# Performance work log

Hardware: AMD Instinct MI355X
Metric: run time of the kernel (lower is better)

Reference implementation:

```python
import jax, jax.numpy as jnp
import numpy as np

D_MODEL = 256
D_FF = 2048
H_HEADS = 8
N_LEVELS = 5
N_POINTS = 4
SPATIAL = [(128, 128), (64, 64), (32, 32), (16, 16), (8, 8)]
LV = sum(h * w for h, w in SPATIAL)  # 21824
LQ = 900
B = 8
D_HEAD = D_MODEL // H_HEADS


def _layer_norm(x, g, b, eps=1e-5):
    m = jnp.mean(x, -1, keepdims=True)
    v = jnp.mean((x - m) ** 2, -1, keepdims=True)
    return (x - m) * jax.lax.rsqrt(v + eps) * g + b


def _ms_deform_core(value, loc, attn_w):
    # value [B,Lv,H,D]; loc [B,Lq,H,L,P,2] normalized in [0,1]; attn_w [B,Lq,H,L,P]
    Bn, Lq = loc.shape[0], loc.shape[1]
    Dh = value.shape[-1]
    out = jnp.zeros((Bn, H_HEADS, Lq, Dh), value.dtype)
    start = 0
    for l, (Hh, Ww) in enumerate(SPATIAL):
        v = value[:, start:start + Hh * Ww].transpose(0, 2, 1, 3)  # [B,H,HW,D]
        start += Hh * Ww
        xy = loc[:, :, :, l]  # [B,Lq,H,P,2]
        # grid_sample align_corners=False: pixel = norm*size - 0.5
        x = xy[..., 0] * Ww - 0.5
        y = xy[..., 1] * Hh - 0.5
        x0 = jnp.floor(x); y0 = jnp.floor(y)
        fx = x - x0; fy = y - y0
        samp = jnp.zeros((Bn, H_HEADS, Lq * N_POINTS, Dh), value.dtype)
        corners = ((0, 0, (1 - fx) * (1 - fy)), (1, 0, fx * (1 - fy)),
                   (0, 1, (1 - fx) * fy), (1, 1, fx * fy))
        for dx, dy, wgt in corners:
            xc = x0 + dx; yc = y0 + dy
            valid = (xc >= 0) & (xc < Ww) & (yc >= 0) & (yc < Hh)  # zero padding
            idx = (jnp.clip(yc, 0, Hh - 1) * Ww + jnp.clip(xc, 0, Ww - 1)).astype(jnp.int32)
            wv = jnp.where(valid, wgt, 0.0)
            idx_r = idx.transpose(0, 2, 1, 3).reshape(Bn, H_HEADS, Lq * N_POINTS)
            wv_r = wv.transpose(0, 2, 1, 3).reshape(Bn, H_HEADS, Lq * N_POINTS)
            g = jnp.take_along_axis(v, idx_r[..., None], axis=2)  # [B,H,LqP,D]
            samp = samp + wv_r[..., None] * g
        samp = samp.reshape(Bn, H_HEADS, Lq, N_POINTS, Dh)
        aw = attn_w[:, :, :, l].transpose(0, 2, 1, 3)  # [B,H,Lq,P]
        out = out + (samp * aw[..., None]).sum(axis=3)
    return out.transpose(0, 2, 1, 3).reshape(Bn, Lq, H_HEADS * Dh)


def _forward(tgt, tgt_query_pos, tgt_reference_points, memory,
             sa_w_q, sa_b_q, sa_w_k, sa_b_k, sa_w_v, sa_b_v, sa_w_o, sa_b_o,
             ca_w_off, ca_b_off, ca_w_attn, ca_b_attn, ca_w_val, ca_b_val, ca_w_out, ca_b_out,
             ffn_w1, ffn_b1, ffn_w2, ffn_b2,
             ln1_g, ln1_b, ln2_g, ln2_b, ln3_g, ln3_b):
    Lq, Bn, C = tgt.shape
    scale = float(1.0 / np.sqrt(D_HEAD))
    # ---- self-attention (torch nn.MultiheadAttention, seq-first) ----
    qk = tgt + tgt_query_pos
    def heads(x):
        return x.reshape(Lq, Bn, H_HEADS, D_HEAD).transpose(1, 2, 0, 3)
    q = heads(qk @ sa_w_q + sa_b_q) * scale
    k = heads(qk @ sa_w_k + sa_b_k)
    v = heads(tgt @ sa_w_v + sa_b_v)
    attn = jax.nn.softmax(jnp.einsum('bhqd,bhkd->bhqk', q, k), axis=-1)
    o = jnp.einsum('bhqk,bhkd->bhqd', attn, v).transpose(2, 0, 1, 3).reshape(Lq, Bn, C)
    tgt = _layer_norm(tgt + (o @ sa_w_o + sa_b_o), ln2_g, ln2_b)
    # ---- multi-scale deformable cross-attention ----
    qb = (tgt + tgt_query_pos).transpose(1, 0, 2)            # [B,Lq,C]
    ref = tgt_reference_points.transpose(1, 0, 2, 3)         # [B,Lq,L,2]
    value = (memory.transpose(1, 0, 2) @ ca_w_val + ca_b_val).reshape(Bn, LV, H_HEADS, D_HEAD)
    off = (qb @ ca_w_off + ca_b_off).reshape(Bn, Lq, H_HEADS, N_LEVELS, N_POINTS, 2)
    aw = jax.nn.softmax((qb @ ca_w_attn + ca_b_attn).reshape(Bn, Lq, H_HEADS, N_LEVELS * N_POINTS), axis=-1)
    aw = aw.reshape(Bn, Lq, H_HEADS, N_LEVELS, N_POINTS)
    offset_normalizer = jnp.asarray([[w, h] for h, w in SPATIAL], tgt.dtype)  # (W,H) per level
    loc = ref[:, :, None, :, None, :] + off / offset_normalizer[None, None, None, :, None, :]
    samp = _ms_deform_core(value, loc, aw)                   # [B,Lq,C]
    o = (samp @ ca_w_out + ca_b_out).transpose(1, 0, 2)
    tgt = _layer_norm(tgt + o, ln1_g, ln1_b)
    # ---- FFN ----
    h = jax.nn.relu(tgt @ ffn_w1 + ffn_b1)
    tgt = _layer_norm(tgt + (h @ ffn_w2 + ffn_b2), ln3_g, ln3_b)
    return tgt


def setup_inputs() -> dict:
    key = jax.random.key(0)
    ks = iter(jax.random.split(key, 64))
    f32 = jnp.float32
    def nrm(shape, s=1.0):
        return (s * jax.random.normal(next(ks), shape)).astype(f32)
    inp = {}
    inp['tgt'] = nrm((LQ, B, D_MODEL))
    inp['tgt_query_pos'] = nrm((LQ, B, D_MODEL))
    inp['tgt_reference_points'] = jax.random.uniform(next(ks), (LQ, B, N_LEVELS, 2), f32)
    inp['memory'] = nrm((LV, B, D_MODEL))
    inp['memory_spatial_shapes'] = jnp.asarray(SPATIAL, jnp.int32)
    inp['memory_level_start_index'] = jnp.asarray(np.cumsum([0] + [h * w for h, w in SPATIAL[:-1]]), jnp.int32)
    for n, shp in [('sa_w_q', (D_MODEL, D_MODEL)), ('sa_w_k', (D_MODEL, D_MODEL)),
                   ('sa_w_v', (D_MODEL, D_MODEL)), ('sa_w_o', (D_MODEL, D_MODEL)),
                   ('ca_w_off', (D_MODEL, H_HEADS * N_LEVELS * N_POINTS * 2)),
                   ('ca_w_attn', (D_MODEL, H_HEADS * N_LEVELS * N_POINTS)),
                   ('ca_w_val', (D_MODEL, D_MODEL)), ('ca_w_out', (D_MODEL, D_MODEL)),
                   ('ffn_w1', (D_MODEL, D_FF)), ('ffn_w2', (D_FF, D_MODEL))]:
        inp[n] = nrm(shp, 0.02)
    for n, d in [('sa_b_q', D_MODEL), ('sa_b_k', D_MODEL), ('sa_b_v', D_MODEL), ('sa_b_o', D_MODEL),
                 ('ca_b_off', H_HEADS * N_LEVELS * N_POINTS * 2), ('ca_b_attn', H_HEADS * N_LEVELS * N_POINTS),
                 ('ca_b_val', D_MODEL), ('ca_b_out', D_MODEL), ('ffn_b1', D_FF), ('ffn_b2', D_MODEL)]:
        inp[n] = jnp.zeros((d,), f32)
    for n in ['ln1', 'ln2', 'ln3']:
        inp[n + '_g'] = jnp.ones((D_MODEL,), f32)
        inp[n + '_b'] = jnp.zeros((D_MODEL,), f32)
    return inp


def reference(tgt, tgt_query_pos, tgt_reference_points, memory,
              memory_spatial_shapes, memory_level_start_index,
              sa_w_q, sa_b_q, sa_w_k, sa_b_k, sa_w_v, sa_b_v, sa_w_o, sa_b_o,
              ca_w_off, ca_b_off, ca_w_attn, ca_b_attn, ca_w_val, ca_b_val, ca_w_out, ca_b_out,
              ffn_w1, ffn_b1, ffn_w2, ffn_b2,
              ln1_g, ln1_b, ln2_g, ln2_b, ln3_g, ln3_b):
    # spatial shapes / level start index are static metadata (SPATIAL), kept for API parity
    return _forward(tgt, tgt_query_pos, tgt_reference_points, memory,
                    sa_w_q, sa_b_q, sa_w_k, sa_b_k, sa_w_v, sa_b_v, sa_w_o, sa_b_o,
                    ca_w_off, ca_b_off, ca_w_attn, ca_b_attn, ca_w_val, ca_b_val, ca_w_out, ca_b_out,
                    ffn_w1, ffn_b1, ffn_w2, ffn_b2,
                    ln1_g, ln1_b, ln2_g, ln2_b, ln3_g, ln3_b)
```

## Files before the change

kernel.cpp:

```cpp
#include <hip/hip_runtime.h>
#include <hip/hip_bf16.h>
#include <type_traits>

#define LQ    900
#define BSZ   8
#define ROWS  (LQ*BSZ)
#define CDIM  256
#define QKS   512
#define OAS   480
#define NH    8
#define DH    32
#define LVTOT 21824
#define VROWS (LVTOT*BSZ)
#define DFF   2048

typedef unsigned short u16;
typedef short short8 __attribute__((ext_vector_type(8)));
typedef float f32x4 __attribute__((ext_vector_type(4)));

__device__ __forceinline__ u16 f2bf(float f) {
    __hip_bfloat16 h = __float2bfloat16(f);
    return *reinterpret_cast<u16*>(&h);
}
#define ATTN_SCALE 0.1767766952966369f
#define SWZ(r) (((r) & 3) ^ (((r) >> 2) & 3))

__global__ __launch_bounds__(256) void addvec_kernel(const float* __restrict__ a,
                                                     const float* __restrict__ b,
                                                     float* __restrict__ c, int n4) {
    int i = blockIdx.x * 256 + threadIdx.x;
    if (i < n4) {
        float4 x = reinterpret_cast<const float4*>(a)[i];
        float4 y = reinterpret_cast<const float4*>(b)[i];
        reinterpret_cast<float4*>(c)[i] = make_float4(x.x+y.x, x.y+y.y, x.z+y.z, x.w+y.w);
    }
}

struct PrepArgs {
    const float* Wq; const float* Wk; const float* Wv; const float* Wo;
    const float* Wval; const float* Wout; const float* Woff; const float* Watt;
    const float* W1; const float* W2;
    u16* WqkT; u16* WvT; u16* WoT; u16* WvalT; u16* WoutT; u16* WoaT; u16* W1T; u16* W2T;
    const float* bq; const float* bk; const float* boff; const float* batt;
    float* bqk; float* boa;
};
__global__ __launch_bounds__(256) void prep_kernel(PrepArgs a) {
    __shared__ float t[32][33];
    const int id = blockIdx.x;
    if (id == 1528) {
        const int tx = threadIdx.x;
        if (tx < 256) { a.bqk[tx] = a.bq[tx] * ATTN_SCALE; a.bqk[256 + tx] = a.bk[tx]; }
        for (int i = tx; i < 320; i += 256) a.boa[i] = a.boff[i];
        if (tx < 160) a.boa[320 + tx] = a.batt[tx];
        return;
    }
    const float* W; u16* Wt; int K = 256, N = 256, nx = 8; float scale = 1.f; int r;
    if      (id < 64)   { W = a.Wq;   Wt = a.WqkT;           scale = ATTN_SCALE; r = id; }
    else if (id < 128)  { W = a.Wk;   Wt = a.WqkT + 256*256; r = id - 64; }
    else if (id < 192)  { W = a.Wv;   Wt = a.WvT;            r = id - 128; }
    else if (id < 256)  { W = a.Wo;   Wt = a.WoT;            r = id - 192; }
    else if (id < 320)  { W = a.Wval; Wt = a.WvalT;          r = id - 256; }
    else if (id < 384)  { W = a.Wout; Wt = a.WoutT;          r = id - 320; }
    else if (id < 464)  { W = a.Woff; Wt = a.WoaT;           N = 320; nx = 10; r = id - 384; }
    else if (id < 504)  { W = a.Watt; Wt = a.WoaT + 320*256; N = 160; nx = 5;  r = id - 464; }
    else if (id < 1016) { W = a.W1;   Wt = a.W1T;            N = 2048; nx = 64; r = id - 504; }
    else                { W = a.W2;   Wt = a.W2T;            K = 2048; N = 256; nx = 8; r = id - 1016; }
    const int n0 = (r % nx) * 32, k0 = (r / nx) * 32;
    const int tx = threadIdx.x & 31, ty = threadIdx.x >> 5;
    #pragma unroll
    for (int rr = ty; rr < 32; rr += 8)
        t[rr][tx] = W[(size_t)(k0 + rr) * N + n0 + tx];
    __syncthreads();
    #pragma unroll
    for (int rr = ty; rr < 32; rr += 8)
        Wt[(size_t)(n0 + rr) * K + k0 + tx] = f2bf(t[tx][rr] * scale);
}

template<typename AT, int RELU, typename OutT>
__device__ __forceinline__ void gemm_body(const AT* __restrict__ A,
                                          const u16* __restrict__ Wt,
                                          const float* __restrict__ bias,
                                          OutT* __restrict__ C,
                                          int M, int N, int K,
                                          int m0, int n0, int tid, u16* S) {
    const int lane = tid & 63;
    const int w = tid >> 6;
    const int wr = w >> 2, wc = w & 3;
    const int lr = lane & 15, lg = lane >> 4;
    const int sr = tid >> 2, sc = tid & 3;
    const int ns = K >> 5;
    const int arow = (m0 + sr < M) ? (m0 + sr) : (M - 1);
    int brow = n0 + sr; if (brow > N - 1) brow = N - 1;
    const u16* Bsrc = Wt + (size_t)brow * K + ((sc ^ SWZ(sr)) << 3);
    u16* Bdst = S + 8192 + ((tid & ~63) << 3);

    f32x4 acc[4][2] = {};
    float4 fal[4], fah[4];
    short8 fab[4];

#define LOADA(I, KK) do { \
    if constexpr (std::is_same<AT, float>::value) { \
        const float4* s_ = reinterpret_cast<const float4*>((const float*)A + (size_t)arow*K + (KK)*32 + sc*8); \
        fal[I] = s_[0]; fah[I] = s_[1]; \
    } else { \
        fab[I] = *reinterpret_cast<const short8*>((const u16*)A + (size_t)arow*K + (KK)*32 + sc*8); \
    } } while (0)

#define STAGEB(BUF, KK) \
    __builtin_amdgcn_global_load_lds((const __attribute__((address_space(1))) void*)(Bsrc + (size_t)(KK)*32), \
        (__attribute__((address_space(3))) void*)(Bdst + (BUF)*4096), 16, 0, 0)

#define WRITEA(BUF, I) do { \
    u16 t_[8]; \
    if constexpr (std::is_same<AT, float>::value) { \
        t_[0]=f2bf(fal[I].x); t_[1]=f2bf(fal[I].y); t_[2]=f2bf(fal[I].z); t_[3]=f2bf(fal[I].w); \
        t_[4]=f2bf(fah[I].x); t_[5]=f2bf(fah[I].y); t_[6]=f2bf(fah[I].z); t_[7]=f2bf(fah[I].w); \
    } else { *reinterpret_cast<short8*>(t_) = fab[I]; } \
    *reinterpret_cast<uint4*>(&S[(BUF)*4096 + sr*32 + ((sc ^ SWZ(sr)) * 8)]) = *reinterpret_cast<const uint4*>(t_); \
    } while (0)

#define WAITVM() do { \
    if constexpr (std::is_same<AT, float>::value) asm volatile("s_waitcnt vmcnt(7)" ::: "memory"); \
    else asm volatile("s_waitcnt vmcnt(5)" ::: "memory"); } while (0)

#define COMPUTE(CUR, BB) do { \
    short8 af_[4], bf_[2]; \
    _Pragma("unroll") for (int i = 0; i < 4; ++i) { \
        const int r_ = wr*64 + i*16 + lr; \
        af_[i] = *reinterpret_cast<const short8*>(&S[(CUR)*4096 + r_*32 + ((lg ^ SWZ(r_)) * 8)]); } \
    _Pragma("unroll") for (int j = 0; j < 2; ++j) { \
        const int rb_ = wc*32 + j*16 + lr; \
        bf_[j] = *reinterpret_cast<const short8*>(&S[8192 + (BB)*4096 + rb_*32 + ((lg ^ SWZ(rb_)) * 8)]); } \
    _Pragma("unroll") for (int i = 0; i < 4; ++i) \
        _Pragma("unroll") for (int j = 0; j < 2; ++j) \
            acc[i][j] = __builtin_amdgcn_mfma_f32_16x16x32_bf16(af_[i], bf_[j], acc[i][j], 0, 0, 0); \
    } while (0)

#define STEP(c) do { \
    asm volatile("s_waitcnt lgkmcnt(0)" ::: "memory"); \
    __builtin_amdgcn_s_barrier(); \
    int kp_ = k4 + (c) + 3; if (kp_ > ns - 1) kp_ = ns - 1; \
    LOADA(((c)+3)&3, kp_); STAGEB(((c)+3)&3, kp_); \
    WAITVM(); \
    WRITEA(((c)+1)&1, ((c)+1)&3); \
    COMPUTE((c)&1, (c)&3); } while (0)

    LOADA(0, 0); STAGEB(0, 0);
    LOADA(1, 1); STAGEB(1, 1);
    LOADA(2, 2); STAGEB(2, 2);
    WAITVM();
    WRITEA(0, 0);

    for (int q = 0; q < (ns >> 2); ++q) {
        const int k4 = q << 2;
        STEP(0); STEP(1); STEP(2); STEP(3);
    }
    asm volatile("s_waitcnt vmcnt(0) lgkmcnt(0)" ::: "memory");
    __builtin_amdgcn_s_barrier();

#undef LOADA
#undef STAGEB
#undef WRITEA
#undef WAITVM
#undef COMPUTE
#undef STEP

    if constexpr (std::is_same<OutT, float>::value) {
        #pragma unroll
        for (int j = 0; j < 2; ++j) {
            const int col = n0 + wc*32 + j*16 + lr;
            if (col >= N) continue;
            const float bcol = bias[col];
            #pragma unroll
            for (int i = 0; i < 4; ++i) {
                #pragma unroll
                for (int r = 0; r < 4; ++r) {
                    const int row = m0 + wr*64 + i*16 + lg*4 + r;
                    if (row >= M) continue;
                    float v = acc[i][j][r] + bcol;
                    if (RELU) v = fmaxf(v, 0.f);
                    C[(size_t)row * N + col] = v;
                }
            }
        }
    } else {
        u16* Ct = S;
        #pragma unroll
        for (int j = 0; j < 2; ++j) {
            const int col = wc*32 + j*16 + lr;
            const float bcol = bias[n0 + col];
            #pragma unroll
            for (int i = 0; i < 4; ++i)
                #pragma unroll
                for (int r = 0; r < 4; ++r) {
                    float v = acc[i][j][r] + bcol;
                    if (RELU) v = fmaxf(v, 0.f);
                    Ct[(wr*64 + i*16 + lg*4 + r)*128 + col] = f2bf(v);
                }
        }
        __syncthreads();
        #pragma unroll
        for (int it = 0; it < 4; ++it) {
            const int idx = it*512 + tid;
            const int row = idx >> 4, cc = idx & 15;
            if (m0 + row < M)
                *reinterpret_cast<uint4*>(&C[(size_t)(m0 + row) * N + n0 + cc*8]) =
                    *reinterpret_cast<const uint4*>(&Ct[row*128 + cc*8]);
        }
    }
}

template<typename AT, int RELU, typename OutT>
__global__ __launch_bounds__(512) void gemm_mfma(const AT* __restrict__ A,
                                                 const u16* __restrict__ Wt,
                                                 const float* __restrict__ bias,
                                                 OutT* __restrict__ C, int M, int N, int K) {
    __shared__ __align__(16) u16 S[24576];
    gemm_body<AT, RELU, OutT>(A, Wt, bias, C, M, N, K,
                              blockIdx.y * 128, blockIdx.x * 128, threadIdx.x, S);
}

__global__ __launch_bounds__(512) void mgemm3_kernel(
        const float* __restrict__ memory, const u16* __restrict__ WvalT, const float* __restrict__ bval, u16* __restrict__ Cval,
        const float* __restrict__ qkin,   const u16* __restrict__ WqkT,  const float* __restrict__ bqk,  u16* __restrict__ Cqk,
        const float* __restrict__ tgtv,   const u16* __restrict__ WvT,   const float* __restrict__ bv,   u16* __restrict__ Cv) {
    __shared__ __align__(16) u16 S[24576];
    int id = blockIdx.x;
    const float* A; const u16* Wt; const float* bias; u16* C; int M, N, m0, n0;
    if (id < 2728)      { A = memory; Wt = WvalT; bias = bval; C = Cval; M = VROWS; N = 256; m0 = (id >> 1)*128; n0 = (id & 1)*128; }
    else if (id < 2956) { id -= 2728; A = qkin; Wt = WqkT; bias = bqk; C = Cqk; M = ROWS; N = 512; m0 = (id >> 2)*128; n0 = (id & 3)*128; }
    else                { id -= 2956; A = tgtv; Wt = WvT; bias = bv; C = Cv; M = ROWS; N = 256; m0 = (id >> 1)*128; n0 = (id & 1)*128; }
    gemm_body<float, 0, u16>(A, Wt, bias, C, M, N, 256, m0, n0, threadIdx.x, S);
}

__global__ __launch_bounds__(256) void attn_mfma_kernel(const u16* __restrict__ qkb,
                                                        const u16* __restrict__ vb,
                                                        float* __restrict__ out) {
    __shared__ __align__(16) u16 Ks[64*32];
    __shared__ __align__(16) u16 Vt[32*64];
    const int bx = blockIdx.x;
    const int qt = bx & 7, h = (bx >> 3) & 7, b = bx >> 6;
    const int tid = threadIdx.x;
    const int w = tid >> 6, lane = tid & 63;
    const int lr = lane & 15, lg = lane >> 4;
    const int m0 = qt*128 + w*32;

    short8 qf[2];
    #pragma unroll
    for (int j = 0; j < 2; ++j) {
        int lq = m0 + j*16 + lr; if (lq > LQ-1) lq = LQ-1;
        qf[j] = *reinterpret_cast<const short8*>(&qkb[((size_t)lq*BSZ + b)*QKS + h*DH + lg*8]);
    }

    f32x4 o00 = {}, o01 = {}, o10 = {}, o11 = {};
    float m[2] = {-1e30f, -1e30f}, l[2] = {0.f, 0.f};
    const f32x4 zero = {};

    for (int kt = 0; kt < 15; ++kt) {
        __syncthreads();
        {
            const int key = tid >> 2, c = tid & 3;
            int kg = kt*64 + key; if (kg > LQ-1) kg = LQ-1;
            *reinterpret_cast<short8*>(&Ks[key*32 + ((c ^ ((key>>1)&3)) * 8)]) =
                *reinterpret_cast<const short8*>(&qkb[((size_t)kg*BSZ + b)*QKS + 256 + h*DH + c*8]);
            short8 vv = *reinterpret_cast<const short8*>(&vb[((size_t)kg*BSZ + b)*CDIM + h*DH + c*8]);
            const u16* pv = reinterpret_cast<const u16*>(&vv);
            #pragma unroll
            for (int e = 0; e < 8; ++e) {
                const int dh = c*8 + e;
                Vt[dh*64 + (((key>>3) ^ (dh&7)) * 8) + (key&7)] = pv[e];
            }
        }
        __syncthreads();

        f32x4 s[4][2];
        #pragma unroll
        for (int i = 0; i < 4; ++i) {
            const int key = i*16 + lr;
            short8 kf = *reinterpret_cast<const short8*>(&Ks[key*32 + ((lg ^ ((key>>1)&3)) * 8)]);
            s[i][0] = __builtin_amdgcn_mfma_f32_16x16x32_bf16(kf, qf[0], zero, 0, 0, 0);
            s[i][1] = __builtin_amdgcn_mfma_f32_16x16x32_bf16(kf, qf[1], zero, 0, 0, 0);
        }
        const int lim = LQ - kt*64 - lg*4;
        #pragma unroll
        for (int i = 0; i < 4; ++i)
            #pragma unroll
            for (int r = 0; r < 4; ++r)
                if (i*16 + r >= lim) { s[i][0][r] = -1e30f; s[i][1][r] = -1e30f; }

        #pragma unroll
        for (int j = 0; j < 2; ++j) {
            float mx = -1e30f;
            #pragma unroll
            for (int i = 0; i < 4; ++i)
                #pragma unroll
                for (int r = 0; r < 4; ++r) mx = fmaxf(mx, s[i][j][r]);
            mx = fmaxf(mx, __shfl_xor(mx, 16));
            mx = fmaxf(mx, __shfl_xor(mx, 32));
            const float mn = fmaxf(m[j], mx);
            const float corr = __expf(m[j] - mn);
            float sum = 0.f;
            #pragma unroll
            for (int i = 0; i < 4; ++i)
                #pragma unroll
                for (int r = 0; r < 4; ++r) {
                    float p = __expf(s[i][j][r] - mn);
                    s[i][j][r] = p;
                    sum += p;
                }
            sum += __shfl_xor(sum, 16);
            sum += __shfl_xor(sum, 32);
            l[j] = l[j]*corr + sum;
            m[j] = mn;
            if (j == 0) { o00 *= corr; o10 *= corr; }
            else        { o01 *= corr; o11 *= corr; }
        }

        short8 pb[2][2];
        #pragma unroll
        for (int kh = 0; kh < 2; ++kh)
            #pragma unroll
            for (int j = 0; j < 2; ++j) {
                u16 t[8];
                #pragma unroll
                for (int e = 0; e < 4; ++e) {
                    t[e]   = f2bf(s[2*kh][j][e]);
                    t[e+4] = f2bf(s[2*kh+1][j][e]);
                }
                pb[kh][j] = *reinterpret_cast<short8*>(t);
            }

        #pragma unroll
        for (int ip = 0; ip < 2; ++ip) {
            const int dh = ip*16 + lr;
            #pragma unroll
            for (int kh = 0; kh < 2; ++kh) {
                u16 t[8];
                const int c0 = (kh*4 + (lg>>1)) ^ (dh&7);
                const int c1 = (kh*4 + 2 + (lg>>1)) ^ (dh&7);
                *reinterpret_cast<uint2*>(&t[0]) =
                    *reinterpret_cast<const uint2*>(&Vt[dh*64 + c0*8 + (lg&1)*4]);
                *reinterpret_cast<uint2*>(&t[4]) =
                    *reinterpret_cast<const uint2*>(&Vt[dh*64 + c1*8 + (lg&1)*4]);
                short8 vf = *reinterpret_cast<short8*>(t);
                if (ip == 0) {
                    o00 = __builtin_amdgcn_mfma_f32_16x16x32_bf16(vf, pb[kh][0], o00, 0, 0, 0);
                    o01 = __builtin_amdgcn_mfma_f32_16x16x32_bf16(vf, pb[kh][1], o01, 0, 0, 0);
                } else {
                    o10 = __builtin_amdgcn_mfma_f32_16x16x32_bf16(vf, pb[kh][0], o10, 0, 0, 0);
                    o11 = __builtin_amdgcn_mfma_f32_16x16x32_bf16(vf, pb[kh][1], o11, 0, 0, 0);
                }
            }
        }
    }

    #pragma unroll
    for (int j = 0; j < 2; ++j) {
        const int lq = m0 + j*16 + lr;
        if (lq >= LQ) continue;
        const float inv = 1.f / l[j];
        float* op = &out[((size_t)lq*BSZ + b)*CDIM + h*DH];
        #pragma unroll
        for (int r = 0; r < 4; ++r) {
            const f32x4& a0 = (j == 0) ? o00 : o01;
            const f32x4& a1 = (j == 0) ? o10 : o11;
            op[lg*4 + r]      = a0[r] * inv;
            op[16 + lg*4 + r] = a1[r] * inv;
        }
    }
}

__global__ __launch_bounds__(256) void ln_res_kernel(const float* __restrict__ xin,
                                                     const float* __restrict__ res,
                                                     const float* __restrict__ g,
                                                     const float* __restrict__ beta,
                                                     float* __restrict__ out) {
    const int row  = blockIdx.x * 4 + (threadIdx.x >> 6);
    const int lane = threadIdx.x & 63;
    const size_t base = (size_t)row * CDIM + lane * 4;
    float4 a = *reinterpret_cast<const float4*>(&xin[base]);
    float4 r = *reinterpret_cast<const float4*>(&res[base]);
    float x0 = a.x+r.x, x1 = a.y+r.y, x2 = a.z+r.z, x3 = a.w+r.w;
    float s = x0+x1+x2+x3;
    #pragma unroll
    for (int o = 1; o < 64; o <<= 1) s += __shfl_xor(s, o);
    float mean = s * (1.f/256.f);
    float d0 = x0-mean, d1 = x1-mean, d2 = x2-mean, d3 = x3-mean;
    float sq = d0*d0 + d1*d1 + d2*d2 + d3*d3;
    #pragma unroll
    for (int o = 1; o < 64; o <<= 1) sq += __shfl_xor(sq, o);
    float rs = rsqrtf(sq * (1.f/256.f) + 1e-5f);
    float4 gg = *reinterpret_cast<const float4*>(&g[lane*4]);
    float4 bb = *reinterpret_cast<const float4*>(&beta[lane*4]);
    float4 o4 = make_float4(d0*rs*gg.x+bb.x, d1*rs*gg.y+bb.y, d2*rs*gg.z+bb.z, d3*rs*gg.w+bb.w);
    *reinterpret_cast<float4*>(&out[base]) = o4;
}

__global__ __launch_bounds__(256) void softmax20_kernel(float* __restrict__ oab) {
    int item = blockIdx.x * 256 + threadIdx.x;
    if (item >= ROWS * NH) return;
    int row = item >> 3, h = item & 7;
    float* p = &oab[(size_t)row*OAS + 320 + h*20];
    float mx = -1e30f;
    float e[20];
    #pragma unroll
    for (int j = 0; j < 20; ++j) mx = fmaxf(mx, p[j]);
    float sum = 0.f;
    #pragma unroll
    for (int j = 0; j < 20; ++j) { e[j] = __expf(p[j] - mx); sum += e[j]; }
    float inv = 1.f / sum;
    #pragma unroll
    for (int j = 0; j < 20; ++j) p[j] = e[j] * inv;
}

__global__ __launch_bounds__(256) void msdeform_kernel(const u16* __restrict__ value,
                                                       const float* __restrict__ oab,
                                                       const float* __restrict__ refp,
                                                       float* __restrict__ samp) {
    const int gid = blockIdx.x * 32 + (threadIdx.x >> 3);
    const int ch  = (threadIdx.x & 7) * 4;
    const int h   = gid & 7;
    const int row = gid >> 3;
    const int b   = row & 7;
    const int WL[5] = {128, 64, 32, 16, 8};
    const int SL[5] = {0, 16384, 20480, 21504, 21760};
    const u16* vbase = value + h*DH + ch;
    float a0 = 0.f, a1 = 0.f, a2 = 0.f, a3 = 0.f;
    #pragma unroll
    for (int l = 0; l < 5; ++l) {
        const float2 r2 = *reinterpret_cast<const float2*>(&refp[((size_t)row*5 + l)*2]);
        const int W = WL[l];
        const float Wf = (float)W;
        #pragma unroll
        for (int p = 0; p < 4; ++p) {
            const float2 o2 = *reinterpret_cast<const float2*>(&oab[(size_t)row*OAS + ((h*5 + l)*4 + p)*2]);
            const float aw = oab[(size_t)row*OAS + 320 + h*20 + l*4 + p];
            const float x = (r2.x + o2.x / Wf) * Wf - 0.5f;
            const float y = (r2.y + o2.y / Wf) * Wf - 0.5f;
            const float x0f = floorf(x), y0f = floorf(y);
            const float fx = x - x0f, fy = y - y0f;
            const int x0 = (int)x0f, y0 = (int)y0f;
            float wx0 = (1.f - fx) * aw, wx1 = fx * aw;
            float fy0 = 1.f - fy, fy1 = fy;
            if (x0 < 0 || x0 >= W)       wx0 = 0.f;
            if (x0+1 < 0 || x0+1 >= W)   wx1 = 0.f;
            if (y0 < 0 || y0 >= W)       fy0 = 0.f;
            if (y0+1 < 0 || y0+1 >= W)   fy1 = 0.f;
            const float w00 = wx0*fy0, w10 = wx1*fy0, w01 = wx0*fy1, w11 = wx1*fy1;
            const int xc0 = min(max(x0, 0), W-1),   xc1 = min(max(x0+1, 0), W-1);
            const int yc0 = min(max(y0, 0), W-1),   yc1 = min(max(y0+1, 0), W-1);
            const int r0 = SL[l] + yc0*W, r1 = SL[l] + yc1*W;
            const int o00i = ((r0 + xc0)*BSZ + b) * CDIM;
            const int o10i = ((r0 + xc1)*BSZ + b) * CDIM;
            const int o01i = ((r1 + xc0)*BSZ + b) * CDIM;
            const int o11i = ((r1 + xc1)*BSZ + b) * CDIM;
            const uint2 u00 = *reinterpret_cast<const uint2*>(vbase + o00i);
            const uint2 u10 = *reinterpret_cast<const uint2*>(vbase + o10i);
            const uint2 u01 = *reinterpret_cast<const uint2*>(vbase + o01i);
            const uint2 u11 = *reinterpret_cast<const uint2*>(vbase + o11i);
            a0 += w00 * __uint_as_float(u00.x << 16) + w10 * __uint_as_float(u10.x << 16)
                + w01 * __uint_as_float(u01.x << 16) + w11 * __uint_as_float(u11.x << 16);
            a1 += w00 * __uint_as_float(u00.x & 0xffff0000u) + w10 * __uint_as_float(u10.x & 0xffff0000u)
                + w01 * __uint_as_float(u01.x & 0xffff0000u) + w11 * __uint_as_float(u11.x & 0xffff0000u);
            a2 += w00 * __uint_as_float(u00.y << 16) + w10 * __uint_as_float(u10.y << 16)
                + w01 * __uint_as_float(u01.y << 16) + w11 * __uint_as_float(u11.y << 16);
            a3 += w00 * __uint_as_float(u00.y & 0xffff0000u) + w10 * __uint_as_float(u10.y & 0xffff0000u)
                + w01 * __uint_as_float(u01.y & 0xffff0000u) + w11 * __uint_as_float(u11.y & 0xffff0000u);
        }
    }
    float4 o4 = make_float4(a0, a1, a2, a3);
    *reinterpret_cast<float4*>(&samp[(size_t)row*CDIM + h*DH + ch]) = o4;
}

extern "C" void kernel_launch(void* const* d_in, const int* in_sizes, int n_in,
                              void* d_out, int out_size, void* d_ws, size_t ws_size,
                              hipStream_t stream) {
    (void)in_sizes; (void)n_in; (void)out_size; (void)ws_size;
    const float* tgt    = (const float*)d_in[0];
    const float* qpos   = (const float*)d_in[1];
    const float* refpts = (const float*)d_in[2];
    const float* memory = (const float*)d_in[3];
    const float* Wq  = (const float*)d_in[6];
    const float* Wk  = (const float*)d_in[7];
    const float* Wv  = (const float*)d_in[8];
    const float* Wo  = (const float*)d_in[9];
    const float* Woff= (const float*)d_in[10];
    const float* Watt= (const float*)d_in[11];
    const float* Wval= (const float*)d_in[12];
    const float* Wout= (const float*)d_in[13];
    const float* W1  = (const float*)d_in[14];
    const float* W2  = (const float*)d_in[15];
    const float* bq  = (const float*)d_in[16];
    const float* bk  = (const float*)d_in[17];
    const float* bv  = (const float*)d_in[18];
    const float* bo  = (const float*)d_in[19];
    const float* boff= (const float*)d_in[20];
    const float* batt= (const float*)d_in[21];
    const float* bval= (const float*)d_in[22];
    const float* bout= (const float*)d_in[23];
    const float* b1  = (const float*)d_in[24];
    const float* b2  = (const float*)d_in[25];
    const float* ln1g= (const float*)d_in[26];
    const float* ln1b= (const float*)d_in[27];
    const float* ln2g= (const float*)d_in[28];
    const float* ln2b= (const float*)d_in[29];
    const float* ln3g= (const float*)d_in[30];
    const float* ln3b= (const float*)d_in[31];
    float* out = (float*)d_out;

    char* ws = (char*)d_ws;
    const size_t RB = (size_t)ROWS * CDIM * 4;
    float* tgt2  = (float*)(ws + 0*RB);
    float* tgt3  = (float*)(ws + 1*RB);
    float* qk    = (float*)(ws + 2*RB);
    float* vbuf  = (float*)(ws + 3*RB);
    float* abuf  = (float*)(ws + 4*RB);
    float* qkin  = (float*)(ws + 5*RB);
    u16* qkb = (u16*)(ws + 6*RB);
    u16* vb  = (u16*)(ws + 6*RB + (size_t)ROWS*QKS*2);
    float* oab = (float*)(ws + 6*RB + (size_t)ROWS*QKS*2 + (size_t)ROWS*CDIM*2);
    char* wsm = ws + 6*RB + (size_t)ROWS*QKS*2 + (size_t)ROWS*CDIM*2 + (size_t)ROWS*OAS*4;
    u16* WqkT  = (u16*)(wsm);
    u16* WvT   = (u16*)(wsm + 262144);
    u16* WoT   = (u16*)(wsm + 262144 + 1*131072);
    u16* WvalT = (u16*)(wsm + 262144 + 2*131072);
    u16* WoutT = (u16*)(wsm + 262144 + 3*131072);
    u16* WoaT  = (u16*)(wsm + 262144 + 4*131072);
    u16* W1T   = (u16*)(wsm + 2*262144 + 4*131072);
    u16* W2T   = (u16*)(wsm + 2*262144 + 4*131072 + 1048576);
    float* bqk = (float*)(wsm + 2*262144 + 4*131072 + 2097152);
    float* boa = (float*)(wsm + 2*262144 + 4*131072 + 2097152 + 2048);
    char* big  = wsm + 2*262144 + 4*131072 + 2097152 + 4096;
    u16* valb  = (u16*)big;
    u16* ffnh  = (u16*)(big + (size_t)VROWS*CDIM*2);

    const dim3 blk(256);
    const dim3 blk512(512);
    const int n4 = ROWS * CDIM / 4;

    PrepArgs pa = { Wq, Wk, Wv, Wo, Wval, Wout, Woff, Watt, W1, W2,
                    WqkT, WvT, WoT, WvalT, WoutT, WoaT, W1T, W2T,
                    bq, bk, boff, batt, bqk, boa };
    prep_kernel<<<dim3(1529), blk, 0, stream>>>(pa);

    addvec_kernel<<<dim3((n4+255)/256), blk, 0, stream>>>(tgt, qpos, qkin, n4);
    mgemm3_kernel<<<dim3(3070), blk512, 0, stream>>>(
        memory, WvalT, bval, valb,
        qkin, WqkT, bqk, qkb,
        tgt, WvT, bv, vb);

    attn_mfma_kernel<<<dim3(512), blk, 0, stream>>>(qkb, vb, abuf);
    gemm_mfma<float,0,float><<<dim3(2,57), blk512, 0, stream>>>(abuf, WoT, bo, qk, ROWS, CDIM, CDIM);
    ln_res_kernel<<<dim3(ROWS/4), blk, 0, stream>>>(qk, tgt, ln2g, ln2b, tgt2);

    addvec_kernel<<<dim3((n4+255)/256), blk, 0, stream>>>(tgt2, qpos, qkin, n4);
    gemm_mfma<float,0,float><<<dim3(4,57), blk512, 0, stream>>>(qkin, WoaT, boa, oab, ROWS, OAS, CDIM);
    softmax20_kernel<<<dim3((ROWS*NH+255)/256), blk, 0, stream>>>(oab);
    msdeform_kernel<<<dim3(ROWS*NH/32), blk, 0, stream>>>(valb, oab, refpts, vbuf);
    gemm_mfma<float,0,float><<<dim3(2,57), blk512, 0, stream>>>(vbuf, WoutT, bout, qk, ROWS, CDIM, CDIM);
    ln_res_kernel<<<dim3(ROWS/4), blk, 0, stream>>>(qk, tgt2, ln1g, ln1b, tgt3);

    gemm_mfma<float,1,u16><<<dim3(16,57), blk512, 0, stream>>>(tgt3, W1T, b1, ffnh, ROWS, DFF, CDIM);
    gemm_mfma<u16,0,float><<<dim3(2,57),  blk512, 0, stream>>>(ffnh, W2T, b2, abuf, ROWS, CDIM, DFF);
    ln_res_kernel<<<dim3(ROWS/4), blk, 0, stream>>>(abuf, tgt3, ln3g, ln3b, out);
}
```

Baseline: 328.3 us.

## Fuse output GEMMs with residual LayerNorm and fold softmax into deform kernel

Adds a 64-row by 256-column GEMM kernel that computes the full output width per block, so the residual add and LayerNorm run in its epilogue. It replaces the three GEMM plus ln_res pairs and drops the intermediate fp32 round trip. The attention softmax is now computed inside the msdeform kernel, which removes a separate kernel and one read-modify-write of oab. It also pads the bf16 epilogue LDS stride to 136 to avoid bank conflicts and reorders value-GEMM block IDs for locality. The fused kernel launches only 113 blocks, which lowers parallelism for the K=2048 FFN2 GEMM.

```diff
diff --git a/kernel.cpp b/kernel.cpp
--- a/kernel.cpp
+++ b/kernel.cpp
@@ -76,6 +76,16 @@
         Wt[(size_t)(n0 + rr) * K + k0 + tx] = f2bf(t[tx][rr] * scale);
 }
 
+__device__ __forceinline__ void stage512(const u16* __restrict__ src, u16* dst,
+                                         int row0, int K, int k0, int maxrow, int tid) {
+    const int sr = tid >> 2, sc = tid & 3;
+    int grow = row0 + sr; if (grow > maxrow) grow = maxrow;
+    const u16* gsrc = src + (size_t)grow * K + k0 + ((sc ^ SWZ(sr)) << 3);
+    u16* ldst = dst + ((tid & ~63) << 3);
+    __builtin_amdgcn_global_load_lds((const __attribute__((address_space(1))) void*)gsrc,
+                                     (__attribute__((address_space(3))) void*)ldst, 16, 0, 0);
+}
+
 template<typename AT, int RELU, typename OutT>
 __device__ __forceinline__ void gemm_body(const AT* __restrict__ A,
                                           const u16* __restrict__ Wt,
@@ -195,7 +205,7 @@
                 for (int r = 0; r < 4; ++r) {
                     float v = acc[i][j][r] + bcol;
                     if (RELU) v = fmaxf(v, 0.f);
-                    Ct[(wr*64 + i*16 + lg*4 + r)*128 + col] = f2bf(v);
+                    Ct[(wr*64 + i*16 + lg*4 + r)*136 + col] = f2bf(v);
                 }
         }
         __syncthreads();
@@ -205,7 +215,7 @@
             const int row = idx >> 4, cc = idx & 15;
             if (m0 + row < M)
                 *reinterpret_cast<uint4*>(&C[(size_t)(m0 + row) * N + n0 + cc*8]) =
-                    *reinterpret_cast<const uint4*>(&Ct[row*128 + cc*8]);
+                    *reinterpret_cast<const uint4*>(&Ct[row*136 + cc*8]);
         }
     }
 }
@@ -226,11 +236,160 @@
         const float* __restrict__ tgtv,   const u16* __restrict__ WvT,   const float* __restrict__ bv,   u16* __restrict__ Cv) {
     __shared__ __align__(16) u16 S[24576];
     int id = blockIdx.x;
-    const float* A; const u16* Wt; const float* bias; u16* C; int M, N, m0, n0;
-    if (id < 2728)      { A = memory; Wt = WvalT; bias = bval; C = Cval; M = VROWS; N = 256; m0 = (id >> 1)*128; n0 = (id & 1)*128; }
-    else if (id < 2956) { id -= 2728; A = qkin; Wt = WqkT; bias = bqk; C = Cqk; M = ROWS; N = 512; m0 = (id >> 2)*128; n0 = (id & 3)*128; }
-    else                { id -= 2956; A = tgtv; Wt = WvT; bias = bv; C = Cv; M = ROWS; N = 256; m0 = (id >> 1)*128; n0 = (id & 1)*128; }
-    gemm_body<float, 0, u16>(A, Wt, bias, C, M, N, 256, m0, n0, threadIdx.x, S);
+    if (id < 2728) {
+        int pair, half;
+        if (id < 2720) { pair = (id >> 4) * 8 + (id & 7); half = (id >> 3) & 1; }
+        else           { int i = id - 2720; pair = 1360 + (i & 3); half = i >> 2; }
+        gemm_body<float, 0, u16>(memory, WvalT, bval, Cval, VROWS, 256, 256,
+                                 pair * 128, half * 128, threadIdx.x, S);
+    } else if (id < 2956) {
+        id -= 2728;
+        gemm_body<float, 0, u16>(qkin, WqkT, bqk, Cqk, ROWS, 512, 256,
+                                 (id >> 2) * 128, (id & 3) * 128, threadIdx.x, S);
+    } else {
+        id -= 2956;
+        gemm_body<float, 0, u16>(tgtv, WvT, bv, Cv, ROWS, 256, 256,
+                                 (id >> 1) * 128, (id & 1) * 128, threadIdx.x, S);
+    }
+}
+
+template<typename AT>
+__global__ __launch_bounds__(512) void gemmln_kernel(const AT* __restrict__ A,
+        const u16* __restrict__ Wt, const float* __restrict__ bias,
+        const float* __restrict__ res, const float* __restrict__ g,
+        const float* __restrict__ beta, float* __restrict__ out,
+        int M, int K) {
+    __shared__ __align__(16) u16 S[20480];
+    const int tid = threadIdx.x;
+    const int lane = tid & 63;
+    const int wv = tid >> 6;
+    const int lr = lane & 15, lg = lane >> 4;
+    const int m0 = blockIdx.x * 64;
+    const int ns = K >> 5;
+    const int asr = tid >> 3, asc = tid & 7;
+    const int afrow = (m0 + asr < M) ? (m0 + asr) : (M - 1);
+    const int bsr = tid >> 2, bsc = tid & 3;
+    const int abrow = (m0 + bsr < M) ? (m0 + bsr) : (M - 1);
+
+    f32x4 acc[4][2] = {};
+    float4 fa;
+
+    auto stageB = [&](int buf, int k0) {
+        stage512(Wt, S + 4096 + buf*8192,        0,   K, k0, 255, tid);
+        stage512(Wt, S + 4096 + buf*8192 + 4096, 128, K, k0, 255, tid);
+    };
+    auto loadA = [&](int k0) {
+        if constexpr (std::is_same<AT, float>::value)
+            fa = *reinterpret_cast<const float4*>((const float*)A + (size_t)afrow*K + k0 + asc*4);
+    };
+    auto putA = [&](int buf, int k0) {
+        if constexpr (std::is_same<AT, float>::value) {
+            u16 t[4] = { f2bf(fa.x), f2bf(fa.y), f2bf(fa.z), f2bf(fa.w) };
+            *reinterpret_cast<uint2*>(&S[buf*2048 + asr*32 + (((asc>>1) ^ SWZ(asr)) * 8) + (asc&1)*4]) =
+                *reinterpret_cast<const uint2*>(t);
+        } else {
+            if (wv < 4) {
+                const u16* gsrc = (const u16*)A + (size_t)abrow*K + k0 + ((bsc ^ SWZ(bsr)) << 3);
+                u16* ldst = S + buf*2048 + ((tid & ~63) << 3);
+                __builtin_amdgcn_global_load_lds((const __attribute__((address_space(1))) void*)gsrc,
+                                                 (__attribute__((address_space(3))) void*)ldst, 16, 0, 0);
+            }
+        }
+    };
+
+    stageB(0, 0);
+    loadA(0);
+    if constexpr (std::is_same<AT, float>::value) putA(0, 0); else putA(0, 0);
+    __syncthreads();
+
+    for (int t = 0; t < ns; ++t) {
+        const int cur = t & 1, nxt = cur ^ 1;
+        if (t + 1 < ns) {
+            stageB(nxt, (t+1) << 5);
+            if constexpr (std::is_same<AT, float>::value) loadA((t+1) << 5);
+            else putA(nxt, (t+1) << 5);
+        }
+        short8 af[4], bf[2];
+        #pragma unroll
+        for (int i = 0; i < 4; ++i) {
+            const int r = i*16 + lr;
+            af[i] = *reinterpret_cast<const short8*>(&S[cur*2048 + r*32 + ((lg ^ SWZ(r)) * 8)]);
+        }
+        #pragma unroll
+        for (int j = 0; j < 2; ++j) {
+            const int rb = wv*32 + j*16 + lr;
+            bf[j] = *reinterpret_cast<const short8*>(&S[4096 + cur*8192 + rb*32 + ((lg ^ SWZ(rb)) * 8)]);
+        }
+        #pragma unroll
+        for (int i = 0; i < 4; ++i)
+            #pragma unroll
+            for (int j = 0; j < 2; ++j)
+                acc[i][j] = __builtin_amdgcn_mfma_f32_16x16x32_bf16(af[i], bf[j], acc[i][j], 0, 0, 0);
+        if (t + 1 < ns) {
+            if constexpr (std::is_same<AT, float>::value) putA(nxt, 0);
+        }
+        __syncthreads();
+    }
+
+    float* P = reinterpret_cast<float*>(S);
+    float* P2 = P + 1024;
+    const float bc0 = bias[wv*32 + lr], bc1 = bias[wv*32 + 16 + lr];
+    #pragma unroll
+    for (int i = 0; i < 4; ++i) {
+        #pragma unroll
+        for (int rr = 0; rr < 4; ++rr) {
+            const int r16 = i*16 + lg*4 + rr;
+            int grow = m0 + r16; if (grow > M - 1) grow = M - 1;
+            float s1 = 0.f, s2 = 0.f;
+            #pragma unroll
+            for (int j = 0; j < 2; ++j) {
+                const int col = wv*32 + j*16 + lr;
+                float v = acc[i][j][rr] + (j ? bc1 : bc0) + res[(size_t)grow*CDIM + col];
+                acc[i][j][rr] = v;
+                s1 += v; s2 += v*v;
+            }
+            #pragma unroll
+            for (int o = 1; o < 16; o <<= 1) {
+                s1 += __shfl_xor(s1, o);
+                s2 += __shfl_xor(s2, o);
+            }
+            if (lr == 0) {
+                P[(r16*8 + wv)*2 + 0] = s1;
+                P[(r16*8 + wv)*2 + 1] = s2;
+            }
+        }
+    }
+    __syncthreads();
+    if (tid < 64) {
+        float s1 = 0.f, s2 = 0.f;
+        #pragma unroll
+        for (int ww = 0; ww < 8; ++ww) {
+            s1 += P[(tid*8 + ww)*2 + 0];
+            s2 += P[(tid*8 + ww)*2 + 1];
+        }
+        const float mean = s1 * (1.f/256.f);
+        const float var  = s2 * (1.f/256.f) - mean*mean;
+        P2[tid*2 + 0] = mean;
+        P2[tid*2 + 1] = rsqrtf(var + 1e-5f);
+    }
+    __syncthreads();
+    const float g0 = g[wv*32 + lr],    g1 = g[wv*32 + 16 + lr];
+    const float e0 = beta[wv*32 + lr], e1 = beta[wv*32 + 16 + lr];
+    #pragma unroll
+    for (int i = 0; i < 4; ++i)
+        #pragma unroll
+        for (int rr = 0; rr < 4; ++rr) {
+            const int r16 = i*16 + lg*4 + rr;
+            const int grow = m0 + r16;
+            if (grow >= M) continue;
+            const float mean = P2[r16*2], rstd = P2[r16*2 + 1];
+            #pragma unroll
+            for (int j = 0; j < 2; ++j) {
+                const int col = wv*32 + j*16 + lr;
+                out[(size_t)grow*CDIM + col] =
+                    (acc[i][j][rr] - mean) * rstd * (j ? g1 : g0) + (j ? e1 : e0);
+            }
+        }
 }
 
 __global__ __launch_bounds__(256) void attn_mfma_kernel(const u16* __restrict__ qkb,
@@ -370,49 +529,6 @@
     }
 }
 
-__global__ __launch_bounds__(256) void ln_res_kernel(const float* __restrict__ xin,
-                                                     const float* __restrict__ res,
-                                                     const float* __restrict__ g,
-                                                     const float* __restrict__ beta,
-                                                     float* __restrict__ out) {
-    const int row  = blockIdx.x * 4 + (threadIdx.x >> 6);
-    const int lane = threadIdx.x & 63;
-    const size_t base = (size_t)row * CDIM + lane * 4;
-    float4 a = *reinterpret_cast<const float4*>(&xin[base]);
-    float4 r = *reinterpret_cast<const float4*>(&res[base]);
-    float x0 = a.x+r.x, x1 = a.y+r.y, x2 = a.z+r.z, x3 = a.w+r.w;
-    float s = x0+x1+x2+x3;
-    #pragma unroll
-    for (int o = 1; o < 64; o <<= 1) s += __shfl_xor(s, o);
-    float mean = s * (1.f/256.f);
-    float d0 = x0-mean, d1 = x1-mean, d2 = x2-mean, d3 = x3-mean;
-    float sq = d0*d0 + d1*d1 + d2*d2 + d3*d3;
-    #pragma unroll
-    for (int o = 1; o < 64; o <<= 1) sq += __shfl_xor(sq, o);
-    float rs = rsqrtf(sq * (1.f/256.f) + 1e-5f);
-    float4 gg = *reinterpret_cast<const float4*>(&g[lane*4]);
-    float4 bb = *reinterpret_cast<const float4*>(&beta[lane*4]);
-    float4 o4 = make_float4(d0*rs*gg.x+bb.x, d1*rs*gg.y+bb.y, d2*rs*gg.z+bb.z, d3*rs*gg.w+bb.w);
-    *reinterpret_cast<float4*>(&out[base]) = o4;
-}
-
-__global__ __launch_bounds__(256) void softmax20_kernel(float* __restrict__ oab) {
-    int item = blockIdx.x * 256 + threadIdx.x;
-    if (item >= ROWS * NH) return;
-    int row = item >> 3, h = item & 7;
-    float* p = &oab[(size_t)row*OAS + 320 + h*20];
-    float mx = -1e30f;
-    float e[20];
-    #pragma unroll
-    for (int j = 0; j < 20; ++j) mx = fmaxf(mx, p[j]);
-    float sum = 0.f;
-    #pragma unroll
-    for (int j = 0; j < 20; ++j) { e[j] = __expf(p[j] - mx); sum += e[j]; }
-    float inv = 1.f / sum;
-    #pragma unroll
-    for (int j = 0; j < 20; ++j) p[j] = e[j] * inv;
-}
-
 __global__ __launch_bounds__(256) void msdeform_kernel(const u16* __restrict__ value,
                                                        const float* __restrict__ oab,
                                                        const float* __restrict__ refp,
@@ -425,6 +541,19 @@
     const int WL[5] = {128, 64, 32, 16, 8};
     const int SL[5] = {0, 16384, 20480, 21504, 21760};
     const u16* vbase = value + h*DH + ch;
+    float e20[20];
+    {
+        const float* sp = &oab[(size_t)row*OAS + 320 + h*20];
+        float mx = -1e30f;
+        #pragma unroll
+        for (int j = 0; j < 20; ++j) { e20[j] = sp[j]; mx = fmaxf(mx, e20[j]); }
+        float sum = 0.f;
+        #pragma unroll
+        for (int j = 0; j < 20; ++j) { e20[j] = __expf(e20[j] - mx); sum += e20[j]; }
+        const float inv = 1.f / sum;
+        #pragma unroll
+        for (int j = 0; j < 20; ++j) e20[j] *= inv;
+    }
     float a0 = 0.f, a1 = 0.f, a2 = 0.f, a3 = 0.f;
     #pragma unroll
     for (int l = 0; l < 5; ++l) {
@@ -434,7 +563,7 @@
         #pragma unroll
         for (int p = 0; p < 4; ++p) {
             const float2 o2 = *reinterpret_cast<const float2*>(&oab[(size_t)row*OAS + ((h*5 + l)*4 + p)*2]);
-            const float aw = oab[(size_t)row*OAS + 320 + h*20 + l*4 + p];
+            const float aw = e20[l*4 + p];
             const float x = (r2.x + o2.x / Wf) * Wf - 0.5f;
             const float y = (r2.y + o2.y / Wf) * Wf - 0.5f;
             const float x0f = floorf(x), y0f = floorf(y);
@@ -512,14 +641,13 @@
     const size_t RB = (size_t)ROWS * CDIM * 4;
     float* tgt2  = (float*)(ws + 0*RB);
     float* tgt3  = (float*)(ws + 1*RB);
-    float* qk    = (float*)(ws + 2*RB);
-    float* vbuf  = (float*)(ws + 3*RB);
-    float* abuf  = (float*)(ws + 4*RB);
-    float* qkin  = (float*)(ws + 5*RB);
-    u16* qkb = (u16*)(ws + 6*RB);
-    u16* vb  = (u16*)(ws + 6*RB + (size_t)ROWS*QKS*2);
-    float* oab = (float*)(ws + 6*RB + (size_t)ROWS*QKS*2 + (size_t)ROWS*CDIM*2);
-    char* wsm = ws + 6*RB + (size_t)ROWS*QKS*2 + (size_t)ROWS*CDIM*2 + (size_t)ROWS*OAS*4;
+    float* vbuf  = (float*)(ws + 2*RB);
+    float* abuf  = (float*)(ws + 3*RB);
+    float* qkin  = (float*)(ws + 4*RB);
+    u16* qkb = (u16*)(ws + 5*RB);
+    u16* vb  = (u16*)(ws + 5*RB + (size_t)ROWS*QKS*2);
+    float* oab = (float*)(ws + 5*RB + (size_t)ROWS*QKS*2 + (size_t)ROWS*CDIM*2);
+    char* wsm = ws + 5*RB + (size_t)ROWS*QKS*2 + (size_t)ROWS*CDIM*2 + (size_t)ROWS*OAS*4;
     u16* WqkT  = (u16*)(wsm);
     u16* WvT   = (u16*)(wsm + 262144);
     u16* WoT   = (u16*)(wsm + 262144 + 1*131072);
@@ -550,17 +678,13 @@
         tgt, WvT, bv, vb);
 
     attn_mfma_kernel<<<dim3(512), blk, 0, stream>>>(qkb, vb, abuf);
-    gemm_mfma<float,0,float><<<dim3(2,57), blk512, 0, stream>>>(abuf, WoT, bo, qk, ROWS, CDIM, CDIM);
-    ln_res_kernel<<<dim3(ROWS/4), blk, 0, stream>>>(qk, tgt, ln2g, ln2b, tgt2);
+    gemmln_kernel<float><<<dim3(113), blk512, 0, stream>>>(abuf, WoT, bo, tgt, ln2g, ln2b, tgt2, ROWS, CDIM);
 
     addvec_kernel<<<dim3((n4+255)/256), blk, 0, stream>>>(tgt2, qpos, qkin, n4);
     gemm_mfma<float,0,float><<<dim3(4,57), blk512, 0, stream>>>(qkin, WoaT, boa, oab, ROWS, OAS, CDIM);
-    softmax20_kernel<<<dim3((ROWS*NH+255)/256), blk, 0, stream>>>(oab);
     msdeform_kernel<<<dim3(ROWS*NH/32), blk, 0, stream>>>(valb, oab, refpts, vbuf);
-    gemm_mfma<float,0,float><<<dim3(2,57), blk512, 0, stream>>>(vbuf, WoutT, bout, qk, ROWS, CDIM, CDIM);
-    ln_res_kernel<<<dim3(ROWS/4), blk, 0, stream>>>(qk, tgt2, ln1g, ln1b, tgt3);
+    gemmln_kernel<float><<<dim3(113), blk512, 0, stream>>>(vbuf, WoutT, bout, tgt2, ln1g, ln1b, tgt3, ROWS, CDIM);
 
     gemm_mfma<float,1,u16><<<dim3(16,57), blk512, 0, stream>>>(tgt3, W1T, b1, ffnh, ROWS, DFF, CDIM);
-    gemm_mfma<u16,0,float><<<dim3(2,57),  blk512, 0, stream>>>(ffnh, W2T, b2, abuf, ROWS, CDIM, DFF);
-    ln_res_kernel<<<dim3(ROWS/4), blk, 0, stream>>>(abuf, tgt3, ln3g, ln3b, out);
-}
+    gemmln_kernel<u16><<<dim3(113), blk512, 0, stream>>>(ffnh, W2T, b2, tgt3, ln3g, ln3b, out, ROWS, DFF);
+}
```

After: 320.9 us. 1.02x faster.
